# Performance work log

Hardware: AMD Instinct MI355X
Metric: run time of the kernel (lower is better)

The kernel has to match this reference:

```python
import jax, jax.numpy as jnp
import numpy as np

# Fixed by module source: forward hardcodes a 200x200 BEV grid, dim=128,
# MSDeformAttn(n_levels=1, n_heads=4, n_points=8).
B, Z, X, C, H, P = 2, 200, 200, 128, 4, 8
N = Z * X
D = C // H  # head dim = 32


def setup_inputs() -> dict:
    key = jax.random.key(0)
    ks = jax.random.split(key, 12)
    s = 0.02
    return {
        "query": jax.random.normal(ks[0], (B, N, C), jnp.float32),
        # MSDeformAttn.value_proj
        "Wv": jax.random.normal(ks[1], (C, C), jnp.float32) * s,
        "bv": jnp.zeros((C,), jnp.float32),
        # MSDeformAttn.sampling_offsets (C -> H*1*P*2)
        "Woff": jax.random.normal(ks[2], (C, H * P * 2), jnp.float32) * s,
        "boff": jax.random.normal(ks[3], (H * P * 2,), jnp.float32) * 2.0,
        # MSDeformAttn.attention_weights (C -> H*1*P)
        "Wattn": jax.random.normal(ks[4], (C, H * P), jnp.float32) * s,
        "battn": jnp.zeros((H * P,), jnp.float32),
        # MSDeformAttn.output_proj
        "Wout1": jax.random.normal(ks[5], (C, C), jnp.float32) * s,
        "bout1": jnp.zeros((C,), jnp.float32),
        # VanillaSelfAttention.output_proj
        "Wout2": jax.random.normal(ks[6], (C, C), jnp.float32) * s,
        "bout2": jnp.zeros((C,), jnp.float32),
    }


def _forward(query, Wv, bv, Woff, boff, Wattn, battn, Wout1, bout1, Wout2, bout2):
    # Reference points: normalized centers of the 200x200 grid, order (z, x).
    zc = (jnp.arange(Z, dtype=jnp.float32) + 0.5) / Z
    xc = (jnp.arange(X, dtype=jnp.float32) + 0.5) / X
    ref = jnp.stack(jnp.meshgrid(zc, xc, indexing="ij"), axis=-1).reshape(N, 2)

    # value_proj on input_flatten (== query); split heads, lay out as images.
    value = (query @ Wv + bv).reshape(B, Z, X, H, D)
    value_flat = value.transpose(0, 3, 1, 2, 4).reshape(B * H, Z * X, D)  # (BH, ZX, D)

    # Sampling locations: ref + offsets / offset_normalizer ([W, H] = [200, 200]).
    off = (query @ Woff + boff).reshape(B, N, H, P, 2)
    norm = jnp.array([X, Z], jnp.float32)
    loc = ref[None, :, None, None, :] + off / norm  # (B, N, H, P, 2)

    # Attention weights: softmax over n_levels*n_points (= P here).
    attn = jax.nn.softmax((query @ Wattn + battn).reshape(B, N, H, P), axis=-1)

    # grid_sample convention: grid = 2*loc - 1, grid[...,0]=x (width), align_corners=False.
    grid = 2.0 * loc - 1.0
    ix = ((grid[..., 0] + 1.0) * X - 1.0) * 0.5  # pixel x coords
    iy = ((grid[..., 1] + 1.0) * Z - 1.0) * 0.5  # pixel y coords
    ix = ix.transpose(0, 2, 1, 3).reshape(B * H, N * P)
    iy = iy.transpose(0, 2, 1, 3).reshape(B * H, N * P)

    x0f = jnp.floor(ix); y0f = jnp.floor(iy)
    lx = ix - x0f; ly = iy - y0f
    x0 = x0f.astype(jnp.int32); y0 = y0f.astype(jnp.int32)
    x1 = x0 + 1; y1 = y0 + 1

    def corner(xi, yi, w):
        # zero padding: out-of-bounds corners contribute 0
        valid = (xi >= 0) & (xi < X) & (yi >= 0) & (yi < Z)
        idx = jnp.clip(yi, 0, Z - 1) * X + jnp.clip(xi, 0, X - 1)  # (BH, N*P)
        v = jnp.take_along_axis(value_flat, idx[..., None], axis=1)  # (BH, N*P, D)
        return v * (w * valid.astype(w.dtype))[..., None]

    sampled = (
        corner(x0, y0, (1.0 - lx) * (1.0 - ly))
        + corner(x1, y0, lx * (1.0 - ly))
        + corner(x0, y1, (1.0 - lx) * ly)
        + corner(x1, y1, lx * ly)
    ).reshape(B, H, N, P, D)

    # Weighted reduce over points, merge heads.
    out = jnp.einsum("bhnpd,bnhp->bnhd", sampled, attn).reshape(B, N, C)
    out = out @ Wout1 + bout1  # MSDeformAttn.output_proj
    out = out @ Wout2 + bout2  # VanillaSelfAttention.output_proj
    return out + query  # dropout is identity in eval; residual add


def reference(query, Wv, bv, Woff, boff, Wattn, battn, Wout1, bout1, Wout2, bout2):
    return _forward(query, Wv, bv, Woff, boff, Wattn, battn, Wout1, bout1, Wout2, bout2)
```

## Files before the change

kernel.cpp:

```cpp
#include <hip/hip_runtime.h>
#include <hip/hip_bf16.h>
#include <cstddef>

namespace {
constexpr int B  = 2;
constexpr int Z  = 200;
constexpr int X  = 200;
constexpr int C  = 128;
constexpr int H  = 4;
constexpr int P  = 8;
constexpr int N  = Z * X;
constexpr int BN = B * N;
constexpr int SC = 128;
constexpr int NF_P = 14;
constexpr int NF_O = 8;
constexpr int KS   = 4;

typedef __attribute__((ext_vector_type(8))) short short8;
typedef __attribute__((ext_vector_type(4))) float f32x4;
typedef _Float16 h16x2 __attribute__((ext_vector_type(2)));

__device__ inline ushort f2bf(float x) {
    __hip_bfloat16 h = __float2bfloat16(x);
    return *reinterpret_cast<ushort*>(&h);
}
__device__ inline unsigned packbf(float a, float b) {
    return (unsigned)f2bf(a) | ((unsigned)f2bf(b) << 16);
}
__device__ inline ushort f2h(float x) {
    _Float16 h = (_Float16)x;
    return __builtin_bit_cast(ushort, h);
}
__device__ inline float h1f(ushort u) {
    return (float)__builtin_bit_cast(_Float16, u);
}
__device__ inline float2 h2f2(unsigned u) {
    h16x2 h = __builtin_bit_cast(h16x2, u);
    return make_float2((float)h[0], (float)h[1]);
}
__device__ inline unsigned packh(float a, float b) {
    return (unsigned)f2h(a) | ((unsigned)f2h(b) << 16);
}
__device__ inline h16x2 pkrtz(float a, float b) {
    return __builtin_bit_cast(h16x2, __builtin_amdgcn_cvt_pkrtz(a, b));
}
template <int MASK>
__device__ inline float swzx(float x) {
    constexpr int pat = (MASK << 10) | 0x1F;
    return __int_as_float(__builtin_amdgcn_ds_swizzle(__float_as_int(x), pat));
}
template <int MASK>
__device__ inline h16x2 swzh(h16x2 x) {
    constexpr int pat = (MASK << 10) | 0x1F;
    int t = __builtin_amdgcn_ds_swizzle(__builtin_bit_cast(int, x), pat);
    return __builtin_bit_cast(h16x2, t);
}
}

__global__ __launch_bounds__(256) void vsa_k_w12(
    const float* __restrict__ Wout1, const float* __restrict__ bout1,
    const float* __restrict__ Wout2, const float* __restrict__ bout2,
    float* __restrict__ w12)
{
    const int c = threadIdx.x & 127;
    const int k = blockIdx.x * 2 + (threadIdx.x >> 7);
    if (k > 128) return;
    const float* arow = (k < 128) ? (Wout1 + (size_t)k * 128) : bout1;
    float acc = (k < 128) ? 0.f : bout2[c];
    #pragma unroll 4
    for (int j = 0; j < 128; ++j)
        acc = fmaf(arow[j], Wout2[(size_t)j * 128 + c], acc);
    w12[(size_t)k * 128 + c] = acc;
}

__global__ __launch_bounds__(256) void vsa_k_prep(
    const float* __restrict__ Wv,    const float* __restrict__ bv,
    const float* __restrict__ Woff,  const float* __restrict__ boff,
    const float* __restrict__ Wattn, const float* __restrict__ battn,
    const float* __restrict__ w12,
    ushort* __restrict__ wtp, ushort* __restrict__ wtp2,
    float* __restrict__ biasp, float* __restrict__ bias2)
{
    const int u = blockIdx.x * 256 + threadIdx.x;
    constexpr int NP = KS * NF_P * 64;
    constexpr int NO = KS * NF_O * 64;

    if (u < NP) {
        int ks  = u / (NF_P * 64);
        int rem = u - ks * (NF_P * 64);
        int f = rem >> 6, l = rem & 63;
        int n  = f * 16 + (l & 15);
        int kb = ks * 32 + (l >> 4) * 8;
        float v[8];
        #pragma unroll
        for (int e = 0; e < 8; ++e) {
            int k = kb + e;
            if (n < 128)      v[e] = Wv[k * 128 + n];
            else if (n < 192) v[e] = Woff[k * 64 + (n - 128)];
            else              v[e] = Wattn[k * 32 + (n - 192)];
        }
        unsigned* dst = (unsigned*)(wtp + (size_t)u * 8);
        #pragma unroll
        for (int i = 0; i < 4; ++i) dst[i] = packbf(v[2*i], v[2*i+1]);
    } else if (u < NP + NO) {
        int t   = u - NP;
        int ks  = t / (NF_O * 64);
        int rem = t - ks * (NF_O * 64);
        int f = rem >> 6, l = rem & 63;
        int n  = f * 16 + (l & 15);
        int kb = ks * 32 + (l >> 4) * 8;
        unsigned* dst = (unsigned*)(wtp2 + (size_t)t * 8);
        #pragma unroll
        for (int i = 0; i < 4; ++i)
            dst[i] = packh(w12[(size_t)(kb + 2*i) * 128 + n],
                           w12[(size_t)(kb + 2*i + 1) * 128 + n]);
    } else if (u < NP + NO + 224) {
        int c = u - NP - NO;
        float bb;
        if (c < 128)      bb = bv[c];
        else if (c < 192) bb = boff[c - 128];
        else              bb = battn[c - 192];
        biasp[c] = bb;
    } else if (u < NP + NO + 224 + 128) {
        int c = u - NP - NO - 224;
        bias2[c] = w12[(size_t)128 * 128 + c];
    }
}

__global__ __launch_bounds__(256) void vsa_k_proj(
    const float* __restrict__ Q, const ushort* __restrict__ wtp,
    const float* __restrict__ biasp,
    ushort* __restrict__ proj_v16, ushort* __restrict__ proj_s16)
{
    const int lane = threadIdx.x & 63;
    const int wave = blockIdx.x * 4 + (threadIdx.x >> 6);
    const int row0 = wave * 16;
    const int m  = lane & 15;
    const int kg = lane >> 4;

    const float* qp = Q + (size_t)(row0 + m) * 128 + kg * 8;

    f32x4 acc[NF_P];
    #pragma unroll
    for (int f = 0; f < NF_P; ++f) acc[f] = (f32x4){0.f, 0.f, 0.f, 0.f};

    #pragma unroll
    for (int ks = 0; ks < KS; ++ks) {
        float4 a0 = *(const float4*)(qp + ks * 32);
        float4 a1 = *(const float4*)(qp + ks * 32 + 4);
        short8 af;
        af[0] = (short)f2bf(a0.x); af[1] = (short)f2bf(a0.y);
        af[2] = (short)f2bf(a0.z); af[3] = (short)f2bf(a0.w);
        af[4] = (short)f2bf(a1.x); af[5] = (short)f2bf(a1.y);
        af[6] = (short)f2bf(a1.z); af[7] = (short)f2bf(a1.w);
        const short8* wrow = (const short8*)wtp + ks * NF_P * 64 + lane;
        #pragma unroll
        for (int f = 0; f < NF_P; ++f)
            acc[f] = __builtin_amdgcn_mfma_f32_16x16x32_bf16(af, wrow[f * 64], acc[f], 0, 0, 0);
    }

    #pragma unroll
    for (int f = 0; f < 8; ++f) {
        const int col = f * 16 + m;
        const float bb = biasp[col];
        #pragma unroll
        for (int r = 0; r < 4; ++r)
            proj_v16[(size_t)(row0 + kg * 4 + r) * 128 + col] = f2h(acc[f][r] + bb);
    }
    #pragma unroll
    for (int f = 8; f < 12; ++f) {
        const int col = f * 16 + m;
        const float bb = biasp[col];
        const int c  = col - 128;
        const int hp = c >> 1, comp = c & 1;
        #pragma unroll
        for (int r = 0; r < 4; ++r)
            proj_s16[(size_t)(row0 + kg * 4 + r) * SC + hp * 4 + comp] = f2h(acc[f][r] + bb);
    }
    #pragma unroll
    for (int f = 12; f < 14; ++f) {
        const float bb = biasp[f * 16 + m];
        const int hp = (f - 12) * 16 + m;
        #pragma unroll
        for (int r = 0; r < 4; ++r) {
            float v = acc[f][r] + bb;
            float mx = v;
            mx = fmaxf(mx, swzx<1>(mx));
            mx = fmaxf(mx, swzx<2>(mx));
            mx = fmaxf(mx, swzx<4>(mx));
            float ex = __expf(v - mx);
            float sm = ex;
            sm += swzx<1>(sm); sm += swzx<2>(sm); sm += swzx<4>(sm);
            const float wp = ex / sm;
            proj_s16[(size_t)(row0 + kg * 4 + r) * SC + hp * 4 + 2] = f2h(wp);
        }
    }
}

__global__ __launch_bounds__(512) void vsa_k_so(
    const ushort* __restrict__ proj_v16, const ushort* __restrict__ proj_s16,
    const ushort* __restrict__ wtp2, const float* __restrict__ bias2,
    const float* __restrict__ Q, float* __restrict__ out)
{
    __shared__ ushort tmp_lds[16][136];

    const int lane = threadIdx.x & 63;
    const int wv   = threadIdx.x >> 6;
    const int hsub = lane >> 5;
    const int p    = (lane >> 2) & 7;
    const int d8   = lane & 3;

    const int orig = blockIdx.x;
    const int wg   = (orig & 7) * 625 + (orig >> 3);
    const int b    = wg / 2500;
    const int bl0  = (wg - b * 2500) * 16;
    const int i0   = bl0 / 200;
    const int j0   = bl0 - i0 * 200;
    const int bn0  = b * N + bl0;

    const ushort* vb = proj_v16 + (size_t)b * N * 128;

    #pragma unroll
    for (int t = 0; t < 4; ++t) {
        const int unit = t * 8 + wv;
        const int pix  = unit >> 1;
        const int h    = (unit & 1) * 2 + hsub;
        const int jr   = j0 + pix;
        const bool wr  = jr >= 200;
        const int i    = i0 + (wr ? 1 : 0);
        const int j    = wr ? jr - 200 : jr;
        const int bn   = bn0 + pix;

        const uint2 ow = *(const uint2*)(proj_s16 + (size_t)bn * SC + (h * 8 + p) * 4);
        const float2 off = h2f2(ow.x);
        const float  wp  = h1f((ushort)(ow.y & 0xffff));

        const float ixf = (float)i + off.x;
        const float iyf = (float)j + off.y;
        const float x0f = floorf(ixf), y0f = floorf(iyf);
        const float lx = ixf - x0f, ly = iyf - y0f;
        const int x0 = (int)x0f, y0 = (int)y0f;
        const int x1 = x0 + 1,  y1 = y0 + 1;
        const int xc0 = min(max(x0, 0), X - 1), xc1 = min(max(x1, 0), X - 1);
        const int yc0 = min(max(y0, 0), Z - 1), yc1 = min(max(y1, 0), Z - 1);

        const float wx0 = ((unsigned)x0 < (unsigned)X) ? (1.f - lx) : 0.f;
        const float wx1 = ((unsigned)x1 < (unsigned)X) ? lx : 0.f;
        const float wy0 = (((unsigned)y0 < (unsigned)Z) ? (1.f - ly) : 0.f) * wp;
        const float wy1 = (((unsigned)y1 < (unsigned)Z) ? ly : 0.f) * wp;

        const h16x2 w00p = pkrtz(wx0 * wy0, wx0 * wy0);
        const h16x2 w10p = pkrtz(wx1 * wy0, wx1 * wy0);
        const h16x2 w01p = pkrtz(wx0 * wy1, wx0 * wy1);
        const h16x2 w11p = pkrtz(wx1 * wy1, wx1 * wy1);

        const int rb0 = yc0 * X, rb1 = yc1 * X;
        const int hb  = h * 32 + d8 * 8;

        const uint4 c00 = *(const uint4*)(vb + (size_t)(rb0 + xc0) * 128 + hb);
        const uint4 c10 = *(const uint4*)(vb + (size_t)(rb0 + xc1) * 128 + hb);
        const uint4 c01 = *(const uint4*)(vb + (size_t)(rb1 + xc0) * 128 + hb);
        const uint4 c11 = *(const uint4*)(vb + (size_t)(rb1 + xc1) * 128 + hb);

        h16x2 a0 = (h16x2)0, a1 = (h16x2)0, a2 = (h16x2)0, a3 = (h16x2)0;
        #define VSA_ACC(c, wpk) { \
            a0 = __builtin_elementwise_fma(__builtin_bit_cast(h16x2, (c).x), wpk, a0); \
            a1 = __builtin_elementwise_fma(__builtin_bit_cast(h16x2, (c).y), wpk, a1); \
            a2 = __builtin_elementwise_fma(__builtin_bit_cast(h16x2, (c).z), wpk, a2); \
            a3 = __builtin_elementwise_fma(__builtin_bit_cast(h16x2, (c).w), wpk, a3); }
        VSA_ACC(c00, w00p)
        VSA_ACC(c10, w10p)
        VSA_ACC(c01, w01p)
        VSA_ACC(c11, w11p)
        #undef VSA_ACC

        a0 += swzh<4>(a0);  a1 += swzh<4>(a1);  a2 += swzh<4>(a2);  a3 += swzh<4>(a3);
        a0 += swzh<8>(a0);  a1 += swzh<8>(a1);  a2 += swzh<8>(a2);  a3 += swzh<8>(a3);
        a0 += swzh<16>(a0); a1 += swzh<16>(a1); a2 += swzh<16>(a2); a3 += swzh<16>(a3);

        if (p == 0) {
            uint4 o;
            o.x = __builtin_bit_cast(unsigned, a0);
            o.y = __builtin_bit_cast(unsigned, a1);
            o.z = __builtin_bit_cast(unsigned, a2);
            o.w = __builtin_bit_cast(unsigned, a3);
            *(uint4*)(&tmp_lds[pix][h * 32 + d8 * 8]) = o;
        }
    }
    __syncthreads();

    const int m  = lane & 15;
    const int kg = lane >> 4;

    f32x4 acc = (f32x4){0.f, 0.f, 0.f, 0.f};
    #pragma unroll
    for (int ks = 0; ks < KS; ++ks) {
        short8 af = *(const short8*)(&tmp_lds[m][ks * 32 + kg * 8]);
        const short8* wrow = (const short8*)wtp2 + ks * NF_O * 64 + lane;
        acc = __builtin_amdgcn_mfma_f32_16x16x32_f16(af, wrow[wv * 64], acc, 0, 0, 0);
    }

    const int col = wv * 16 + m;
    const float bb = bias2[col];
    #pragma unroll
    for (int r = 0; r < 4; ++r) {
        const size_t gi = (size_t)(bn0 + kg * 4 + r) * 128 + col;
        const float q = __builtin_nontemporal_load(Q + gi);
        __builtin_nontemporal_store(acc[r] + bb + q, out + gi);
    }
}

extern "C" void kernel_launch(void* const* d_in, const int* in_sizes, int n_in,
                              void* d_out, int out_size, void* d_ws, size_t ws_size,
                              hipStream_t stream) {
    const float* Q     = (const float*)d_in[0];
    const float* Wv    = (const float*)d_in[1];
    const float* bv    = (const float*)d_in[2];
    const float* Woff  = (const float*)d_in[3];
    const float* boff  = (const float*)d_in[4];
    const float* Wattn = (const float*)d_in[5];
    const float* battn = (const float*)d_in[6];
    const float* Wout1 = (const float*)d_in[7];
    const float* bout1 = (const float*)d_in[8];
    const float* Wout2 = (const float*)d_in[9];
    const float* bout2 = (const float*)d_in[10];
    float* out = (float*)d_out;

    float*  biasp  = (float*)d_ws;
    float*  bias2  = biasp + 224;
    float*  w12    = bias2 + 128;
    ushort* proj_s16 = (ushort*)(w12 + 129 * 128);
    ushort* proj_v16 = proj_s16 + (size_t)BN * SC;
    ushort* wtp    = proj_v16 + (size_t)BN * 128;
    ushort* wtp2   = wtp + (size_t)KS * NF_P * 64 * 8;

    constexpr int prep_n = KS * NF_P * 64 + KS * NF_O * 64 + 224 + 128;
    vsa_k_w12<<<65, 256, 0, stream>>>(Wout1, bout1, Wout2, bout2, w12);
    vsa_k_prep<<<(prep_n + 255) / 256, 256, 0, stream>>>(
        Wv, bv, Woff, boff, Wattn, battn, w12, wtp, wtp2, biasp, bias2);
    vsa_k_proj<<<BN / 64, 256, 0, stream>>>(Q, wtp, biasp, proj_v16, proj_s16);
    vsa_k_so<<<BN / 16, 512, 0, stream>>>(proj_v16, proj_s16, wtp2, bias2, Q, out);
}
```

Measured before the change: 92.62 us.

## Fold point reduction into MFMA via LDS planes and transpose MFMA outputs

The sampling kernel no longer reduces the eight points with cross-lane swizzles. Each point writes its partial result to its own LDS plane, and the output projection sums over the points by running extra MFMAs over the planes. Both kernels swap the MFMA operand order so each lane holds four contiguous columns, which permits vectorised bias loads and packed half stores, and the softmax needs only one swizzle. The LDS footprint grows to about 35 KB and the MFMA count rises eightfold, which may lower occupancy, and the residual query load is issued before the barrier.

```diff
diff --git a/kernel.cpp b/kernel.cpp
--- a/kernel.cpp
+++ b/kernel.cpp
@@ -15,6 +15,7 @@
 constexpr int NF_P = 14;
 constexpr int NF_O = 8;
 constexpr int KS   = 4;
+constexpr int PLANE = 2200;
 
 typedef __attribute__((ext_vector_type(8))) short short8;
 typedef __attribute__((ext_vector_type(4))) float f32x4;
@@ -48,12 +49,6 @@
 __device__ inline float swzx(float x) {
     constexpr int pat = (MASK << 10) | 0x1F;
     return __int_as_float(__builtin_amdgcn_ds_swizzle(__float_as_int(x), pat));
-}
-template <int MASK>
-__device__ inline h16x2 swzh(h16x2 x) {
-    constexpr int pat = (MASK << 10) | 0x1F;
-    int t = __builtin_amdgcn_ds_swizzle(__builtin_bit_cast(int, x), pat);
-    return __builtin_bit_cast(h16x2, t);
 }
 }
 
@@ -156,44 +151,46 @@
         const short8* wrow = (const short8*)wtp + ks * NF_P * 64 + lane;
         #pragma unroll
         for (int f = 0; f < NF_P; ++f)
-            acc[f] = __builtin_amdgcn_mfma_f32_16x16x32_bf16(af, wrow[f * 64], acc[f], 0, 0, 0);
-    }
+            acc[f] = __builtin_amdgcn_mfma_f32_16x16x32_bf16(wrow[f * 64], af, acc[f], 0, 0, 0);
+    }
+
+    const size_t rb = (size_t)(row0 + m);
 
     #pragma unroll
     for (int f = 0; f < 8; ++f) {
-        const int col = f * 16 + m;
-        const float bb = biasp[col];
-        #pragma unroll
-        for (int r = 0; r < 4; ++r)
-            proj_v16[(size_t)(row0 + kg * 4 + r) * 128 + col] = f2h(acc[f][r] + bb);
+        const int col0 = f * 16 + kg * 4;
+        const float4 bb = *(const float4*)(biasp + col0);
+        uint2 o;
+        o.x = packh(acc[f][0] + bb.x, acc[f][1] + bb.y);
+        o.y = packh(acc[f][2] + bb.z, acc[f][3] + bb.w);
+        *(uint2*)(proj_v16 + rb * 128 + col0) = o;
     }
     #pragma unroll
     for (int f = 8; f < 12; ++f) {
-        const int col = f * 16 + m;
-        const float bb = biasp[col];
-        const int c  = col - 128;
-        const int hp = c >> 1, comp = c & 1;
-        #pragma unroll
-        for (int r = 0; r < 4; ++r)
-            proj_s16[(size_t)(row0 + kg * 4 + r) * SC + hp * 4 + comp] = f2h(acc[f][r] + bb);
+        const int col0 = f * 16 + kg * 4;
+        const float4 bb = *(const float4*)(biasp + col0);
+        const int hp0 = (col0 - 128) >> 1;
+        *(unsigned*)(proj_s16 + rb * SC + hp0 * 4)       = packh(acc[f][0] + bb.x, acc[f][1] + bb.y);
+        *(unsigned*)(proj_s16 + rb * SC + (hp0 + 1) * 4) = packh(acc[f][2] + bb.z, acc[f][3] + bb.w);
     }
     #pragma unroll
     for (int f = 12; f < 14; ++f) {
-        const float bb = biasp[f * 16 + m];
-        const int hp = (f - 12) * 16 + m;
-        #pragma unroll
-        for (int r = 0; r < 4; ++r) {
-            float v = acc[f][r] + bb;
-            float mx = v;
-            mx = fmaxf(mx, swzx<1>(mx));
-            mx = fmaxf(mx, swzx<2>(mx));
-            mx = fmaxf(mx, swzx<4>(mx));
-            float ex = __expf(v - mx);
-            float sm = ex;
-            sm += swzx<1>(sm); sm += swzx<2>(sm); sm += swzx<4>(sm);
-            const float wp = ex / sm;
-            proj_s16[(size_t)(row0 + kg * 4 + r) * SC + hp * 4 + 2] = f2h(wp);
-        }
+        const int col0 = f * 16 + kg * 4;
+        const float4 bb = *(const float4*)(biasp + col0);
+        float v0 = acc[f][0] + bb.x, v1 = acc[f][1] + bb.y;
+        float v2 = acc[f][2] + bb.z, v3 = acc[f][3] + bb.w;
+        float mx = fmaxf(fmaxf(v0, v1), fmaxf(v2, v3));
+        mx = fmaxf(mx, swzx<16>(mx));
+        const float e0 = __expf(v0 - mx), e1 = __expf(v1 - mx);
+        const float e2 = __expf(v2 - mx), e3 = __expf(v3 - mx);
+        float sm = e0 + e1 + e2 + e3;
+        sm += swzx<16>(sm);
+        const float inv = 1.0f / sm;
+        const int c0 = col0 - 192;
+        proj_s16[rb * SC + (c0 + 0) * 4 + 2] = f2h(e0 * inv);
+        proj_s16[rb * SC + (c0 + 1) * 4 + 2] = f2h(e1 * inv);
+        proj_s16[rb * SC + (c0 + 2) * 4 + 2] = f2h(e2 * inv);
+        proj_s16[rb * SC + (c0 + 3) * 4 + 2] = f2h(e3 * inv);
     }
 }
 
@@ -202,7 +199,7 @@
     const ushort* __restrict__ wtp2, const float* __restrict__ bias2,
     const float* __restrict__ Q, float* __restrict__ out)
 {
-    __shared__ ushort tmp_lds[16][136];
+    __shared__ ushort tmp_lds[P * PLANE];
 
     const int lane = threadIdx.x & 63;
     const int wv   = threadIdx.x >> 6;
@@ -220,23 +217,29 @@
 
     const ushort* vb = proj_v16 + (size_t)b * N * 128;
 
+    int pix_t[4], h_t[4];
+    float fi_t[4], fj_t[4];
+    uint2 ow[4];
     #pragma unroll
     for (int t = 0; t < 4; ++t) {
         const int unit = t * 8 + wv;
         const int pix  = unit >> 1;
-        const int h    = (unit & 1) * 2 + hsub;
+        pix_t[t] = pix;
+        h_t[t]   = (unit & 1) * 2 + hsub;
         const int jr   = j0 + pix;
         const bool wr  = jr >= 200;
-        const int i    = i0 + (wr ? 1 : 0);
-        const int j    = wr ? jr - 200 : jr;
-        const int bn   = bn0 + pix;
-
-        const uint2 ow = *(const uint2*)(proj_s16 + (size_t)bn * SC + (h * 8 + p) * 4);
-        const float2 off = h2f2(ow.x);
-        const float  wp  = h1f((ushort)(ow.y & 0xffff));
-
-        const float ixf = (float)i + off.x;
-        const float iyf = (float)j + off.y;
+        fi_t[t] = (float)(i0 + (wr ? 1 : 0));
+        fj_t[t] = (float)(wr ? jr - 200 : jr);
+        ow[t] = *(const uint2*)(proj_s16 + (size_t)(bn0 + pix) * SC + (h_t[t] * 8 + p) * 4);
+    }
+
+    #pragma unroll
+    for (int t = 0; t < 4; ++t) {
+        const float2 off = h2f2(ow[t].x);
+        const float  wp  = h1f((ushort)(ow[t].y & 0xffff));
+
+        const float ixf = fi_t[t] + off.x;
+        const float iyf = fj_t[t] + off.y;
         const float x0f = floorf(ixf), y0f = floorf(iyf);
         const float lx = ixf - x0f, ly = iyf - y0f;
         const int x0 = (int)x0f, y0 = (int)y0f;
@@ -255,7 +258,7 @@
         const h16x2 w11p = pkrtz(wx1 * wy1, wx1 * wy1);
 
         const int rb0 = yc0 * X, rb1 = yc1 * X;
-        const int hb  = h * 32 + d8 * 8;
+        const int hb  = h_t[t] * 32 + d8 * 8;
 
         const uint4 c00 = *(const uint4*)(vb + (size_t)(rb0 + xc0) * 128 + hb);
         const uint4 c10 = *(const uint4*)(vb + (size_t)(rb0 + xc1) * 128 + hb);
@@ -274,40 +277,36 @@
         VSA_ACC(c11, w11p)
         #undef VSA_ACC
 
-        a0 += swzh<4>(a0);  a1 += swzh<4>(a1);  a2 += swzh<4>(a2);  a3 += swzh<4>(a3);
-        a0 += swzh<8>(a0);  a1 += swzh<8>(a1);  a2 += swzh<8>(a2);  a3 += swzh<8>(a3);
-        a0 += swzh<16>(a0); a1 += swzh<16>(a1); a2 += swzh<16>(a2); a3 += swzh<16>(a3);
-
-        if (p == 0) {
-            uint4 o;
-            o.x = __builtin_bit_cast(unsigned, a0);
-            o.y = __builtin_bit_cast(unsigned, a1);
-            o.z = __builtin_bit_cast(unsigned, a2);
-            o.w = __builtin_bit_cast(unsigned, a3);
-            *(uint4*)(&tmp_lds[pix][h * 32 + d8 * 8]) = o;
+        uint4 o;
+        o.x = __builtin_bit_cast(unsigned, a0);
+        o.y = __builtin_bit_cast(unsigned, a1);
+        o.z = __builtin_bit_cast(unsigned, a2);
+        o.w = __builtin_bit_cast(unsigned, a3);
+        *(uint4*)(&tmp_lds[p * PLANE + pix_t[t] * 136 + h_t[t] * 32 + d8 * 8]) = o;
+    }
+
+    const int m   = lane & 15;
+    const int kg  = lane >> 4;
+    const int col0 = wv * 16 + kg * 4;
+    const f32x4 qv = __builtin_nontemporal_load(
+        (const f32x4*)(Q + (size_t)(bn0 + m) * 128 + col0));
+
+    __syncthreads();
+
+    f32x4 acc = (f32x4){0.f, 0.f, 0.f, 0.f};
+    #pragma unroll
+    for (int ks = 0; ks < KS; ++ks) {
+        const short8 wfrag = ((const short8*)wtp2)[ks * NF_O * 64 + wv * 64 + lane];
+        #pragma unroll
+        for (int pp = 0; pp < P; ++pp) {
+            const short8 af = *(const short8*)(&tmp_lds[pp * PLANE + m * 136 + ks * 32 + kg * 8]);
+            acc = __builtin_amdgcn_mfma_f32_16x16x32_f16(wfrag, af, acc, 0, 0, 0);
         }
     }
-    __syncthreads();
-
-    const int m  = lane & 15;
-    const int kg = lane >> 4;
-
-    f32x4 acc = (f32x4){0.f, 0.f, 0.f, 0.f};
-    #pragma unroll
-    for (int ks = 0; ks < KS; ++ks) {
-        short8 af = *(const short8*)(&tmp_lds[m][ks * 32 + kg * 8]);
-        const short8* wrow = (const short8*)wtp2 + ks * NF_O * 64 + lane;
-        acc = __builtin_amdgcn_mfma_f32_16x16x32_f16(af, wrow[wv * 64], acc, 0, 0, 0);
-    }
-
-    const int col = wv * 16 + m;
-    const float bb = bias2[col];
-    #pragma unroll
-    for (int r = 0; r < 4; ++r) {
-        const size_t gi = (size_t)(bn0 + kg * 4 + r) * 128 + col;
-        const float q = __builtin_nontemporal_load(Q + gi);
-        __builtin_nontemporal_store(acc[r] + bb + q, out + gi);
-    }
+
+    const f32x4 bb = *(const f32x4*)(bias2 + col0);
+    f32x4 o = acc + bb + qv;
+    __builtin_nontemporal_store(o, (f32x4*)(out + (size_t)(bn0 + m) * 128 + col0));
 }
 
 extern "C" void kernel_launch(void* const* d_in, const int* in_sizes, int n_in,
```

Measured after the change: 109.3 us. 18.0% more time.

## Store value projection in zero-padded bordered image to drop bounds checks

Applied to the files above, without the earlier changes.

The value projection is written into a zero-bordered image with a 24-pixel border and a 256-wide row pitch. The border is zeroed by extra blocks in the weight-fusion kernel. Bilinear sampling then clamps coordinates into the padded range and reads four corners at fixed byte offsets, with no per-corner validity masks or index clamps. The head-to-wave mapping is fixed per wave, and the residual Q load is hoisted ahead of the barrier. The cost is a larger workspace, extra zeroing writes, and offsets beyond the border are clamped rather than sampled.

```diff
diff --git a/kernel.cpp b/kernel.cpp
--- a/kernel.cpp
+++ b/kernel.cpp
@@ -15,6 +15,10 @@
 constexpr int NF_P = 14;
 constexpr int NF_O = 8;
 constexpr int KS   = 4;
+constexpr int PW   = 256;
+constexpr int PH   = 248;
+constexpr int BORD = 24;
+constexpr size_t VB_STRIDE = (size_t)PH * PW * 128;
 
 typedef __attribute__((ext_vector_type(8))) short short8;
 typedef __attribute__((ext_vector_type(4))) float f32x4;
@@ -57,11 +61,27 @@
 }
 }
 
-__global__ __launch_bounds__(256) void vsa_k_w12(
+__global__ __launch_bounds__(256) void vsa_k_w12b(
     const float* __restrict__ Wout1, const float* __restrict__ bout1,
     const float* __restrict__ Wout2, const float* __restrict__ bout2,
-    float* __restrict__ w12)
+    float* __restrict__ w12, ushort* __restrict__ proj_vp)
 {
+    if (blockIdx.x >= 65) {
+        const int bid2 = blockIdx.x - 65;
+        const int bb = bid2 / PH, Y = bid2 - bb * PH;
+        const bool borderRow = (Y < BORD) || (Y >= PH - BORD);
+        int px = -1;
+        if (borderRow) px = threadIdx.x;
+        else if (threadIdx.x < 2 * BORD)
+            px = (threadIdx.x < BORD) ? (int)threadIdx.x : (int)threadIdx.x + (PW - 2 * BORD);
+        if (px >= 0) {
+            uint4* dst = (uint4*)(proj_vp + (size_t)bb * VB_STRIDE + ((size_t)Y * PW + px) * 128);
+            const uint4 z = {0u, 0u, 0u, 0u};
+            #pragma unroll
+            for (int q = 0; q < 16; ++q) dst[q] = z;
+        }
+        return;
+    }
     const int c = threadIdx.x & 127;
     const int k = blockIdx.x * 2 + (threadIdx.x >> 7);
     if (k > 128) return;
@@ -130,7 +150,7 @@
 __global__ __launch_bounds__(256) void vsa_k_proj(
     const float* __restrict__ Q, const ushort* __restrict__ wtp,
     const float* __restrict__ biasp,
-    ushort* __restrict__ proj_v16, ushort* __restrict__ proj_s16)
+    ushort* __restrict__ proj_vp, ushort* __restrict__ proj_s16)
 {
     const int lane = threadIdx.x & 63;
     const int wave = blockIdx.x * 4 + (threadIdx.x >> 6);
@@ -159,31 +179,44 @@
             acc[f] = __builtin_amdgcn_mfma_f32_16x16x32_bf16(af, wrow[f * 64], acc[f], 0, 0, 0);
     }
 
+    const int bb  = row0 / 40000;
+    const int lcl = row0 - bb * 40000;
+    const int y0p = lcl / 200;
+    const int x0p = lcl - y0p * 200;
+    size_t prow[4];
+    #pragma unroll
+    for (int r = 0; r < 4; ++r) {
+        const int idx = kg * 4 + r;
+        int xr = x0p + idx, yr = y0p;
+        if (xr >= 200) { xr -= 200; yr += 1; }
+        prow[r] = (size_t)bb * VB_STRIDE + (((size_t)(yr + BORD) * PW) + (xr + BORD)) * 128;
+    }
+
     #pragma unroll
     for (int f = 0; f < 8; ++f) {
         const int col = f * 16 + m;
-        const float bb = biasp[col];
+        const float bbv = biasp[col];
         #pragma unroll
         for (int r = 0; r < 4; ++r)
-            proj_v16[(size_t)(row0 + kg * 4 + r) * 128 + col] = f2h(acc[f][r] + bb);
+            proj_vp[prow[r] + col] = f2h(acc[f][r] + bbv);
     }
     #pragma unroll
     for (int f = 8; f < 12; ++f) {
         const int col = f * 16 + m;
-        const float bb = biasp[col];
+        const float bbv = biasp[col];
         const int c  = col - 128;
         const int hp = c >> 1, comp = c & 1;
         #pragma unroll
         for (int r = 0; r < 4; ++r)
-            proj_s16[(size_t)(row0 + kg * 4 + r) * SC + hp * 4 + comp] = f2h(acc[f][r] + bb);
+            proj_s16[(size_t)(row0 + kg * 4 + r) * SC + hp * 4 + comp] = f2h(acc[f][r] + bbv);
     }
     #pragma unroll
     for (int f = 12; f < 14; ++f) {
-        const float bb = biasp[f * 16 + m];
+        const float bbv = biasp[f * 16 + m];
         const int hp = (f - 12) * 16 + m;
         #pragma unroll
         for (int r = 0; r < 4; ++r) {
-            float v = acc[f][r] + bb;
+            float v = acc[f][r] + bbv;
             float mx = v;
             mx = fmaxf(mx, swzx<1>(mx));
             mx = fmaxf(mx, swzx<2>(mx));
@@ -198,7 +231,7 @@
 }
 
 __global__ __launch_bounds__(512) void vsa_k_so(
-    const ushort* __restrict__ proj_v16, const ushort* __restrict__ proj_s16,
+    const ushort* __restrict__ proj_vp, const ushort* __restrict__ proj_s16,
     const ushort* __restrict__ wtp2, const float* __restrict__ bias2,
     const float* __restrict__ Q, float* __restrict__ out)
 {
@@ -209,6 +242,8 @@
     const int hsub = lane >> 5;
     const int p    = (lane >> 2) & 7;
     const int d8   = lane & 3;
+    const int h    = (wv & 1) * 2 + hsub;
+    const int hb   = h * 64 + d8 * 16;
 
     const int orig = blockIdx.x;
     const int wg   = (orig & 7) * 625 + (orig >> 3);
@@ -218,49 +253,40 @@
     const int j0   = bl0 - i0 * 200;
     const int bn0  = b * N + bl0;
 
-    const ushort* vb = proj_v16 + (size_t)b * N * 128;
+    const char* vbp = (const char*)(proj_vp + (size_t)b * VB_STRIDE);
 
     #pragma unroll
     for (int t = 0; t < 4; ++t) {
-        const int unit = t * 8 + wv;
-        const int pix  = unit >> 1;
-        const int h    = (unit & 1) * 2 + hsub;
+        const int pix  = t * 4 + (wv >> 1);
         const int jr   = j0 + pix;
         const bool wr  = jr >= 200;
-        const int i    = i0 + (wr ? 1 : 0);
-        const int j    = wr ? jr - 200 : jr;
+        const float fi = (float)(i0 + (wr ? 1 : 0));
+        const float fj = (float)(wr ? jr - 200 : jr);
         const int bn   = bn0 + pix;
 
         const uint2 ow = *(const uint2*)(proj_s16 + (size_t)bn * SC + (h * 8 + p) * 4);
         const float2 off = h2f2(ow.x);
         const float  wp  = h1f((ushort)(ow.y & 0xffff));
 
-        const float ixf = (float)i + off.x;
-        const float iyf = (float)j + off.y;
+        const float ixf = fminf(fmaxf(fi + off.x, -23.f), 222.f);
+        const float iyf = fminf(fmaxf(fj + off.y, -23.f), 222.f);
         const float x0f = floorf(ixf), y0f = floorf(iyf);
         const float lx = ixf - x0f, ly = iyf - y0f;
-        const int x0 = (int)x0f, y0 = (int)y0f;
-        const int x1 = x0 + 1,  y1 = y0 + 1;
-        const int xc0 = min(max(x0, 0), X - 1), xc1 = min(max(x1, 0), X - 1);
-        const int yc0 = min(max(y0, 0), Z - 1), yc1 = min(max(y1, 0), Z - 1);
-
-        const float wx0 = ((unsigned)x0 < (unsigned)X) ? (1.f - lx) : 0.f;
-        const float wx1 = ((unsigned)x1 < (unsigned)X) ? lx : 0.f;
-        const float wy0 = (((unsigned)y0 < (unsigned)Z) ? (1.f - ly) : 0.f) * wp;
-        const float wy1 = (((unsigned)y1 < (unsigned)Z) ? ly : 0.f) * wp;
-
-        const h16x2 w00p = pkrtz(wx0 * wy0, wx0 * wy0);
-        const h16x2 w10p = pkrtz(wx1 * wy0, wx1 * wy0);
-        const h16x2 w01p = pkrtz(wx0 * wy1, wx0 * wy1);
-        const h16x2 w11p = pkrtz(wx1 * wy1, wx1 * wy1);
-
-        const int rb0 = yc0 * X, rb1 = yc1 * X;
-        const int hb  = h * 32 + d8 * 8;
-
-        const uint4 c00 = *(const uint4*)(vb + (size_t)(rb0 + xc0) * 128 + hb);
-        const uint4 c10 = *(const uint4*)(vb + (size_t)(rb0 + xc1) * 128 + hb);
-        const uint4 c01 = *(const uint4*)(vb + (size_t)(rb1 + xc0) * 128 + hb);
-        const uint4 c11 = *(const uint4*)(vb + (size_t)(rb1 + xc1) * 128 + hb);
+        const int Xp = (int)x0f + BORD;
+        const int Yp = (int)y0f + BORD;
+
+        const float wy0 = (1.f - ly) * wp;
+        const float wy1 = ly * wp;
+        const h16x2 w00p = pkrtz((1.f - lx) * wy0, (1.f - lx) * wy0);
+        const h16x2 w10p = pkrtz(lx * wy0, lx * wy0);
+        const h16x2 w01p = pkrtz((1.f - lx) * wy1, (1.f - lx) * wy1);
+        const h16x2 w11p = pkrtz(lx * wy1, lx * wy1);
+
+        const char* base = vbp + ((((size_t)Yp << 8) + Xp) << 8) + hb;
+        const uint4 c00 = *(const uint4*)(base);
+        const uint4 c10 = *(const uint4*)(base + 256);
+        const uint4 c01 = *(const uint4*)(base + 65536);
+        const uint4 c11 = *(const uint4*)(base + 65536 + 256);
 
         h16x2 a0 = (h16x2)0, a1 = (h16x2)0, a2 = (h16x2)0, a3 = (h16x2)0;
         #define VSA_ACC(c, wpk) { \
@@ -287,10 +313,16 @@
             *(uint4*)(&tmp_lds[pix][h * 32 + d8 * 8]) = o;
         }
     }
-    __syncthreads();
 
     const int m  = lane & 15;
     const int kg = lane >> 4;
+    const int col = wv * 16 + m;
+    float qv[4];
+    #pragma unroll
+    for (int r = 0; r < 4; ++r)
+        qv[r] = __builtin_nontemporal_load(Q + (size_t)(bn0 + kg * 4 + r) * 128 + col);
+
+    __syncthreads();
 
     f32x4 acc = (f32x4){0.f, 0.f, 0.f, 0.f};
     #pragma unroll
@@ -300,13 +332,11 @@
         acc = __builtin_amdgcn_mfma_f32_16x16x32_f16(af, wrow[wv * 64], acc, 0, 0, 0);
     }
 
-    const int col = wv * 16 + m;
     const float bb = bias2[col];
     #pragma unroll
     for (int r = 0; r < 4; ++r) {
         const size_t gi = (size_t)(bn0 + kg * 4 + r) * 128 + col;
-        const float q = __builtin_nontemporal_load(Q + gi);
-        __builtin_nontemporal_store(acc[r] + bb + q, out + gi);
+        __builtin_nontemporal_store(acc[r] + bb + qv[r], out + gi);
     }
 }
 
@@ -330,14 +360,14 @@
     float*  bias2  = biasp + 224;
     float*  w12    = bias2 + 128;
     ushort* proj_s16 = (ushort*)(w12 + 129 * 128);
-    ushort* proj_v16 = proj_s16 + (size_t)BN * SC;
-    ushort* wtp    = proj_v16 + (size_t)BN * 128;
+    ushort* proj_vp  = proj_s16 + (size_t)BN * SC;
+    ushort* wtp    = proj_vp + 2 * VB_STRIDE;
     ushort* wtp2   = wtp + (size_t)KS * NF_P * 64 * 8;
 
     constexpr int prep_n = KS * NF_P * 64 + KS * NF_O * 64 + 224 + 128;
-    vsa_k_w12<<<65, 256, 0, stream>>>(Wout1, bout1, Wout2, bout2, w12);
+    vsa_k_w12b<<<65 + 2 * PH, 256, 0, stream>>>(Wout1, bout1, Wout2, bout2, w12, proj_vp);
     vsa_k_prep<<<(prep_n + 255) / 256, 256, 0, stream>>>(
         Wv, bv, Woff, boff, Wattn, battn, w12, wtp, wtp2, biasp, bias2);
-    vsa_k_proj<<<BN / 64, 256, 0, stream>>>(Q, wtp, biasp, proj_v16, proj_s16);
-    vsa_k_so<<<BN / 16, 512, 0, stream>>>(proj_v16, proj_s16, wtp2, bias2, Q, out);
-}
+    vsa_k_proj<<<BN / 64, 256, 0, stream>>>(Q, wtp, biasp, proj_vp, proj_s16);
+    vsa_k_so<<<BN / 16, 512, 0, stream>>>(proj_vp, proj_s16, wtp2, bias2, Q, out);
+}
```

Measured after the change: 101.2 us. 9.2% more time.
